# Kernel tuning notes

Hardware: AMD Instinct MI355X
Metric: run time of the kernel (lower is better)

Reference implementation:

```python
import jax, jax.numpy as jnp
import numpy as np

D = 32        # number of TT cores (d)
R = 16        # tt_rank
B = 262144    # batch size


def setup_inputs() -> dict:
    key = jax.random.key(0)
    k1, k2, k3, k4 = jax.random.split(key, 4)
    return {
        "X": jax.random.randint(k1, (B, D), 0, 2, dtype=jnp.int32),
        "core_first": jax.random.normal(k2, (1, R, 2), dtype=jnp.float32),
        "cores_mid": jax.random.normal(k3, (D - 2, R, R, 2), dtype=jnp.float32),
        "core_last": jax.random.normal(k4, (R, 1, 2), dtype=jnp.float32),
    }


def reference(X, core_first, cores_mid, core_last):
    # First core: cores[0][:, :, X[:,0]] -> [1, R, B] -> permute -> [B, 1, R].
    # We carry the squeezed [B, R] row vector instead of [B, 1, R].
    carry0 = jnp.take(core_first[0], X[:, 0], axis=-1).T  # [B, R]

    def step(carry, inp):
        core, idx = inp                       # core: [R, R, 2], idx: [B]
        c = jnp.take(core, idx, axis=2)       # gathered core: [R, R, B]
        new = jnp.einsum('br,rsb->bs', carry, c)  # batched (1xR)@(RxR)
        return new, None

    # Middle cores i = 1 .. D-2 (sequential chain, data-dependent).
    carry, _ = jax.lax.scan(step, carry0, (cores_mid, X[:, 1:D - 1].T))

    # Last core: cores[-1][:, :, X[:,-1]] -> [R, 1, B]; contract to scalar per batch.
    c_last = jnp.take(core_last[:, 0, :], X[:, -1], axis=-1)  # [R, B]
    out = jnp.einsum('br,rb->b', carry, c_last)               # [B]  (squeeze of [B,1,1])
    return out
```

## Files before the change

### kernel.cpp

```cpp
#include <hip/hip_runtime.h>


#define R 16
#define TT_D 32
#define BATCH 262144

#define OFF_V8   0
#define OFF_P8   (OFF_V8 + 4096)
#define OFF_Q8   (OFF_P8 + 65536)
#define OFF_W8   (OFF_Q8 + 65536)
#define OFF_V16  (OFF_W8 + 4096)
#define OFF_W16  (OFF_V16 + 1048576)
#define WS_FLOATS (OFF_W16 + 1048576)

typedef int   v4i __attribute__((ext_vector_type(4)));
typedef float v4f __attribute__((ext_vector_type(4)));
typedef float v2f __attribute__((ext_vector_type(2)));

__device__ inline void row_chain4(const float* __restrict__ Lc, int cbase, int e, int r,
                                  float* __restrict__ v) {
    const int b0 = (e >> 3) & 1, b1 = (e >> 2) & 1, b2 = (e >> 1) & 1, b3 = e & 1;
    #pragma unroll
    for (int s = 0; s < 16; s++) v[s] = Lc[((((cbase * 2 + b0) * 16) + s) << 4) + r];
    const int bits[3] = { b1, b2, b3 };
    #pragma unroll
    for (int k = 1; k <= 3; k++) {
        const float* M = Lc + (((cbase + k) * 2 + bits[k - 1]) << 8);
        float nv[16];
        #pragma unroll
        for (int s2 = 0; s2 < 16; s2++) {
            float acc = 0.f;
            #pragma unroll
            for (int r2 = 0; r2 < 16; r2++) acc += v[r2] * M[(s2 << 4) + r2];
            nv[s2] = acc;
        }
        #pragma unroll
        for (int s2 = 0; s2 < 16; s2++) v[s2] = nv[s2];
    }
}

__global__ __launch_bounds__(256) void tt_build1(const float* __restrict__ cf,
                                                 const float* __restrict__ cm,
                                                 const float* __restrict__ cl,
                                                 float* __restrict__ ws) {
    __shared__ float sh[12288];
    const int g = blockIdx.x;
    const int t = threadIdx.x;

    if (g < 32) {
        const bool isP = (g < 16);
        const int gb = isP ? g : g - 16;
        const int coreBase = isP ? 7 : 15;
        for (int i = t; i < 8 * 512; i += 256) {
            const int c = i >> 9, j = i & 511;
            const int x = j & 1, s = (j >> 1) & 15, r = j >> 5;
            sh[(((c * 2 + x) * 16) + s) * 16 + r] = cm[coreBase * 512 + i];
        }
        __syncthreads();
        {
            const int e = t >> 4, r = t & 15;
            float v[16];
            row_chain4(sh, 4, e, r, v);
            #pragma unroll
            for (int s = 0; s < 16; s++) sh[8192 + (e << 8) + (r << 4) + s] = v[s];
        }
        if (t < 16) {
            float v[16];
            row_chain4(sh, 0, gb, t, v);
            #pragma unroll
            for (int s = 0; s < 16; s++) sh[4096 + (t << 4) + s] = v[s];
        }
        __syncthreads();
        {
            const int l = t >> 4, r = t & 15;
            float h[16], outv[16];
            #pragma unroll
            for (int k = 0; k < 16; k++) h[k] = sh[4096 + (r << 4) + k];
            #pragma unroll
            for (int s2 = 0; s2 < 16; s2++) outv[s2] = 0.f;
            #pragma unroll
            for (int k = 0; k < 16; k++) {
                const float a = h[k];
                #pragma unroll
                for (int s2 = 0; s2 < 16; s2++) outv[s2] += a * sh[8192 + (l << 8) + (k << 4) + s2];
            }
            const int e8 = gb * 16 + l;
            float* o = ws + (isP ? OFF_P8 : OFF_Q8) + (e8 << 8) + (r << 4);
            #pragma unroll
            for (int s2 = 0; s2 < 16; s2++) o[s2] = outv[s2];
        }
    } else if (g == 32) {
        for (int i = t; i < 7 * 512; i += 256) {
            const int c = i >> 9, j = i & 511;
            const int x = j & 1, s = (j >> 1) & 15, r = j >> 5;
            sh[(((c * 2 + x) * 16) + s) * 16 + r] = cm[i];
        }
        if (t < 32) sh[8192 + t] = cf[t];
        __syncthreads();
        {
            const int e = t >> 4, r = t & 15;
            float v[16];
            row_chain4(sh, 3, e, r, v);
            #pragma unroll
            for (int s = 0; s < 16; s++) sh[4096 + (e << 8) + (r << 4) + s] = v[s];
        }
        if (t < 16) {
            const int e = t;
            const int b0 = (e >> 3) & 1, b1 = (e >> 2) & 1, b2 = (e >> 1) & 1, b3 = e & 1;
            float v[16];
            #pragma unroll
            for (int s = 0; s < 16; s++) v[s] = sh[8192 + s * 2 + b0];
            const int bits[3] = { b1, b2, b3 };
            #pragma unroll
            for (int k = 1; k <= 3; k++) {
                const float* M = sh + (((k - 1) * 2 + bits[k - 1]) << 8);
                float nv[16];
                #pragma unroll
                for (int s2 = 0; s2 < 16; s2++) {
                    float acc = 0.f;
                    #pragma unroll
                    for (int r2 = 0; r2 < 16; r2++) acc += v[r2] * M[(s2 << 4) + r2];
                    nv[s2] = acc;
                }
                #pragma unroll
                for (int s2 = 0; s2 < 16; s2++) v[s2] = nv[s2];
            }
            #pragma unroll
            for (int s = 0; s < 16; s++) sh[8256 + (e << 4) + s] = v[s];
        }
        __syncthreads();
        {
            const int h = t >> 4, l = t & 15;
            float outv[16];
            #pragma unroll
            for (int s2 = 0; s2 < 16; s2++) outv[s2] = 0.f;
            #pragma unroll
            for (int k = 0; k < 16; k++) {
                const float a = sh[8256 + (h << 4) + k];
                #pragma unroll
                for (int s2 = 0; s2 < 16; s2++) outv[s2] += a * sh[4096 + (l << 8) + (k << 4) + s2];
            }
            float* o = ws + OFF_V8 + (t << 4);
            #pragma unroll
            for (int s2 = 0; s2 < 16; s2++) o[s2] = outv[s2];
        }
    } else {
        for (int i = t; i < 7 * 512; i += 256) {
            const int c = i >> 9, j = i & 511;
            const int x = j & 1, s = (j >> 1) & 15, r = j >> 5;
            sh[(((c * 2 + x) * 16) + s) * 16 + r] = cm[23 * 512 + i];
        }
        if (t < 32) sh[8192 + t] = cl[t];
        __syncthreads();
        {
            const int e = t >> 4, r = t & 15;
            float v[16];
            row_chain4(sh, 0, e, r, v);
            #pragma unroll
            for (int s = 0; s < 16; s++) sh[4096 + (e << 8) + (r << 4) + s] = v[s];
        }
        if (t < 16) {
            const int e = t;
            const int b0 = (e >> 3) & 1, b1 = (e >> 2) & 1, b2 = (e >> 1) & 1, b3 = e & 1;
            float w[16];
            #pragma unroll
            for (int r2 = 0; r2 < 16; r2++) w[r2] = sh[8192 + r2 * 2 + b3];
            const int cidx[3] = { 6, 5, 4 };
            const int bidx[3] = { b2, b1, b0 };
            #pragma unroll
            for (int k = 0; k < 3; k++) {
                const float* M = sh + ((cidx[k] * 2 + bidx[k]) << 8);
                float nw[16];
                #pragma unroll
                for (int r2 = 0; r2 < 16; r2++) {
                    float acc = 0.f;
                    #pragma unroll
                    for (int kk = 0; kk < 16; kk++) acc += M[(kk << 4) + r2] * w[kk];
                    nw[r2] = acc;
                }
                #pragma unroll
                for (int r2 = 0; r2 < 16; r2++) w[r2] = nw[r2];
            }
            #pragma unroll
            for (int r2 = 0; r2 < 16; r2++) sh[8256 + (e << 4) + r2] = w[r2];
        }
        __syncthreads();
        {
            const int h = t >> 4, l = t & 15;
            float w4[16], outv[16];
            #pragma unroll
            for (int k = 0; k < 16; k++) w4[k] = sh[8256 + (l << 4) + k];
            #pragma unroll
            for (int r2 = 0; r2 < 16; r2++) {
                float acc = 0.f;
                #pragma unroll
                for (int k = 0; k < 16; k++) acc += sh[4096 + (h << 8) + (r2 << 4) + k] * w4[k];
                outv[r2] = acc;
            }
            float* o = ws + OFF_W8 + (t << 4);
            #pragma unroll
            for (int r2 = 0; r2 < 16; r2++) o[r2] = outv[r2];
        }
    }
}

__global__ __launch_bounds__(256) void tt_build2(float* __restrict__ ws) {
    const int t = threadIdx.x;
    if (blockIdx.x < 256) {
        const int h = blockIdx.x, l = t;
        __shared__ float sv[16];
        if (t < 16) sv[t] = ws[OFF_V8 + h * 16 + t];
        __syncthreads();
        const float* P = ws + OFF_P8 + (l << 8);
        float outv[16];
        #pragma unroll
        for (int s2 = 0; s2 < 16; s2++) outv[s2] = 0.f;
        #pragma unroll
        for (int r2 = 0; r2 < 16; r2++) {
            const float a = sv[r2];
            #pragma unroll
            for (int s2 = 0; s2 < 16; s2++) outv[s2] += a * P[(r2 << 4) + s2];
        }
        float* o = ws + OFF_V16 + (size_t)((h << 8) + l) * 16;
        #pragma unroll
        for (int s2 = 0; s2 < 16; s2++) o[s2] = outv[s2];
    } else {
        const int h = blockIdx.x - 256, l = t;
        __shared__ float sQ[256];
        sQ[t] = ws[OFF_Q8 + (h << 8) + t];
        __syncthreads();
        const float* wv = ws + OFF_W8 + (l << 4);
        float w[16];
        #pragma unroll
        for (int k = 0; k < 16; k++) w[k] = wv[k];
        float outv[16];
        #pragma unroll
        for (int r2 = 0; r2 < 16; r2++) {
            float acc = 0.f;
            #pragma unroll
            for (int k = 0; k < 16; k++) acc += sQ[(r2 << 4) + k] * w[k];
            outv[r2] = acc;
        }
        float* o = ws + OFF_W16 + (size_t)((h << 8) + l) * 16;
        #pragma unroll
        for (int r2 = 0; r2 < 16; r2++) o[r2] = outv[r2];
    }
}

__global__ __launch_bounds__(256) void tt_main2(const int* __restrict__ X,
                                                const float* __restrict__ ws,
                                                float* __restrict__ out) {
    const int tid = blockIdx.x * 256 + threadIdx.x;
    const v4i* Xr = (const v4i*)(X + (size_t)tid * 64);
    v4i c[16];
    #pragma unroll
    for (int q = 0; q < 16; q++) c[q] = __builtin_nontemporal_load(Xr + q);

    unsigned key[4] = { 0u, 0u, 0u, 0u };
    #pragma unroll
    for (int q = 0; q < 16; q++) {
        const unsigned nib = ((unsigned)(c[q].x & 1) << 3) | ((unsigned)(c[q].y & 1) << 2) |
                             ((unsigned)(c[q].z & 1) << 1) | (unsigned)(c[q].w & 1);
        key[q >> 2] = (key[q >> 2] << 4) | nib;
    }

    const v4f* v0 = (const v4f*)(ws + OFF_V16 + (size_t)key[0] * 16);
    const v4f* w0 = (const v4f*)(ws + OFF_W16 + (size_t)key[1] * 16);
    const v4f* v1 = (const v4f*)(ws + OFF_V16 + (size_t)key[2] * 16);
    const v4f* w1 = (const v4f*)(ws + OFF_W16 + (size_t)key[3] * 16);

    v4f acc0 = { 0.f, 0.f, 0.f, 0.f }, acc1 = { 0.f, 0.f, 0.f, 0.f };
    #pragma unroll
    for (int k = 0; k < 4; k++) acc0 += v0[k] * w0[k];
    #pragma unroll
    for (int k = 0; k < 4; k++) acc1 += v1[k] * w1[k];

    v2f res;
    res.x = acc0.x + acc0.y + acc0.z + acc0.w;
    res.y = acc1.x + acc1.y + acc1.z + acc1.w;
    __builtin_nontemporal_store(res, (v2f*)(out + (size_t)tid * 2));
}

__global__ __launch_bounds__(256) void tt_direct(const int* __restrict__ X,
                                                 const float* __restrict__ cf,
                                                 const float* __restrict__ cm,
                                                 const float* __restrict__ cl,
                                                 float* __restrict__ out) {
    __shared__ float scm[30 * 16 * 16 * 2];
    for (int i = threadIdx.x; i < 30 * 16 * 16 * 2; i += blockDim.x) scm[i] = cm[i];
    __syncthreads();
    const int b = blockIdx.x * blockDim.x + threadIdx.x;
    if (b >= BATCH) return;
    const int* xr = X + (size_t)b * TT_D;
    float v[R], nv[R];
    const int x0 = xr[0] & 1;
    #pragma unroll
    for (int r = 0; r < R; r++) v[r] = cf[r * 2 + x0];
    for (int i = 1; i <= 30; i++) {
        const int bit = xr[i] & 1;
        const float* M = scm + (i - 1) * 512;
        #pragma unroll
        for (int s2 = 0; s2 < R; s2++) {
            float acc = 0.f;
            #pragma unroll
            for (int r = 0; r < R; r++) acc += v[r] * M[(r * 16 + s2) * 2 + bit];
            nv[s2] = acc;
        }
        #pragma unroll
        for (int s2 = 0; s2 < R; s2++) v[s2] = nv[s2];
    }
    const int xl = xr[31] & 1;
    float acc = 0.f;
    #pragma unroll
    for (int r = 0; r < R; r++) acc += v[r] * cl[r * 2 + xl];
    out[b] = acc;
}

extern "C" void kernel_launch(void* const* d_in, const int* in_sizes, int n_in,
                              void* d_out, int out_size, void* d_ws, size_t ws_size,
                              hipStream_t stream) {
    const int* X = (const int*)d_in[0];
    const float* cf = (const float*)d_in[1];
    const float* cm = (const float*)d_in[2];
    const float* cl = (const float*)d_in[3];
    float* out = (float*)d_out;

    if (ws_size >= (size_t)WS_FLOATS * sizeof(float)) {
        float* ws = (float*)d_ws;
        tt_build1<<<34, 256, 0, stream>>>(cf, cm, cl, ws);
        tt_build2<<<512, 256, 0, stream>>>(ws);
        tt_main2<<<BATCH / 512, 256, 0, stream>>>(X, ws, out);
    } else {
        tt_direct<<<(BATCH + 255) / 256, 256, 0, stream>>>(X, cf, cm, cl, out);
    }
}
```

Before: 135.1 us.

## Rebuild 8-core byte tables with one block per table entry

The table-building stage moves from 34 large blocks, each doing serial nibble chains in a big shared buffer, to 544 small blocks. Each block computes one 8-core product directly as a chain of 16x16 matrix steps, one thread per output element, reading cores straight from global memory. The second stage is rearranged so each block holds one P matrix in shared memory and loops over the V8 vectors. The aim is to shorten the latency of the build phase by filling more compute units, at the cost of more redundant global reads and a barrier at every chain step.

```diff
diff --git a/kernel.cpp b/kernel.cpp
--- a/kernel.cpp
+++ b/kernel.cpp
@@ -17,233 +17,124 @@
 typedef float v4f __attribute__((ext_vector_type(4)));
 typedef float v2f __attribute__((ext_vector_type(2)));
 
-__device__ inline void row_chain4(const float* __restrict__ Lc, int cbase, int e, int r,
-                                  float* __restrict__ v) {
-    const int b0 = (e >> 3) & 1, b1 = (e >> 2) & 1, b2 = (e >> 1) & 1, b3 = e & 1;
-    #pragma unroll
-    for (int s = 0; s < 16; s++) v[s] = Lc[((((cbase * 2 + b0) * 16) + s) << 4) + r];
-    const int bits[3] = { b1, b2, b3 };
-    #pragma unroll
-    for (int k = 1; k <= 3; k++) {
-        const float* M = Lc + (((cbase + k) * 2 + bits[k - 1]) << 8);
-        float nv[16];
-        #pragma unroll
-        for (int s2 = 0; s2 < 16; s2++) {
-            float acc = 0.f;
-            #pragma unroll
-            for (int r2 = 0; r2 < 16; r2++) acc += v[r2] * M[(s2 << 4) + r2];
-            nv[s2] = acc;
-        }
-        #pragma unroll
-        for (int s2 = 0; s2 < 16; s2++) v[s2] = nv[s2];
-    }
-}
-
-__global__ __launch_bounds__(256) void tt_build1(const float* __restrict__ cf,
-                                                 const float* __restrict__ cm,
-                                                 const float* __restrict__ cl,
-                                                 float* __restrict__ ws) {
-    __shared__ float sh[12288];
+__global__ __launch_bounds__(256) void tt_byte_build(const float* __restrict__ cf,
+                                                     const float* __restrict__ cm,
+                                                     const float* __restrict__ cl,
+                                                     float* __restrict__ ws) {
+    __shared__ float sA[256], sB[256];
     const int g = blockIdx.x;
     const int t = threadIdx.x;
 
-    if (g < 32) {
-        const bool isP = (g < 16);
-        const int gb = isP ? g : g - 16;
-        const int coreBase = isP ? 7 : 15;
-        for (int i = t; i < 8 * 512; i += 256) {
-            const int c = i >> 9, j = i & 511;
-            const int x = j & 1, s = (j >> 1) & 15, r = j >> 5;
-            sh[(((c * 2 + x) * 16) + s) * 16 + r] = cm[coreBase * 512 + i];
-        }
-        __syncthreads();
+    if (g < 512) {
+        const bool isP = (g < 256);
+        const int e = g & 255;
+        const int base = isP ? 7 : 15;
+        const int r = t >> 4, s = t & 15;
         {
-            const int e = t >> 4, r = t & 15;
-            float v[16];
-            row_chain4(sh, 4, e, r, v);
-            #pragma unroll
-            for (int s = 0; s < 16; s++) sh[8192 + (e << 8) + (r << 4) + s] = v[s];
-        }
-        if (t < 16) {
-            float v[16];
-            row_chain4(sh, 0, gb, t, v);
-            #pragma unroll
-            for (int s = 0; s < 16; s++) sh[4096 + (t << 4) + s] = v[s];
-        }
-        __syncthreads();
-        {
-            const int l = t >> 4, r = t & 15;
-            float h[16], outv[16];
-            #pragma unroll
-            for (int k = 0; k < 16; k++) h[k] = sh[4096 + (r << 4) + k];
-            #pragma unroll
-            for (int s2 = 0; s2 < 16; s2++) outv[s2] = 0.f;
-            #pragma unroll
-            for (int k = 0; k < 16; k++) {
-                const float a = h[k];
-                #pragma unroll
-                for (int s2 = 0; s2 < 16; s2++) outv[s2] += a * sh[8192 + (l << 8) + (k << 4) + s2];
-            }
-            const int e8 = gb * 16 + l;
-            float* o = ws + (isP ? OFF_P8 : OFF_Q8) + (e8 << 8) + (r << 4);
-            #pragma unroll
-            for (int s2 = 0; s2 < 16; s2++) o[s2] = outv[s2];
-        }
-    } else if (g == 32) {
-        for (int i = t; i < 7 * 512; i += 256) {
-            const int c = i >> 9, j = i & 511;
-            const int x = j & 1, s = (j >> 1) & 15, r = j >> 5;
-            sh[(((c * 2 + x) * 16) + s) * 16 + r] = cm[i];
-        }
-        if (t < 32) sh[8192 + t] = cf[t];
-        __syncthreads();
-        {
-            const int e = t >> 4, r = t & 15;
-            float v[16];
-            row_chain4(sh, 3, e, r, v);
-            #pragma unroll
-            for (int s = 0; s < 16; s++) sh[4096 + (e << 8) + (r << 4) + s] = v[s];
-        }
-        if (t < 16) {
-            const int e = t;
-            const int b0 = (e >> 3) & 1, b1 = (e >> 2) & 1, b2 = (e >> 1) & 1, b3 = e & 1;
-            float v[16];
-            #pragma unroll
-            for (int s = 0; s < 16; s++) v[s] = sh[8192 + s * 2 + b0];
-            const int bits[3] = { b1, b2, b3 };
-            #pragma unroll
-            for (int k = 1; k <= 3; k++) {
-                const float* M = sh + (((k - 1) * 2 + bits[k - 1]) << 8);
-                float nv[16];
-                #pragma unroll
-                for (int s2 = 0; s2 < 16; s2++) {
-                    float acc = 0.f;
-                    #pragma unroll
-                    for (int r2 = 0; r2 < 16; r2++) acc += v[r2] * M[(s2 << 4) + r2];
-                    nv[s2] = acc;
-                }
-                #pragma unroll
-                for (int s2 = 0; s2 < 16; s2++) v[s2] = nv[s2];
-            }
-            #pragma unroll
-            for (int s = 0; s < 16; s++) sh[8256 + (e << 4) + s] = v[s];
-        }
-        __syncthreads();
-        {
-            const int h = t >> 4, l = t & 15;
-            float outv[16];
-            #pragma unroll
-            for (int s2 = 0; s2 < 16; s2++) outv[s2] = 0.f;
-            #pragma unroll
-            for (int k = 0; k < 16; k++) {
-                const float a = sh[8256 + (h << 4) + k];
-                #pragma unroll
-                for (int s2 = 0; s2 < 16; s2++) outv[s2] += a * sh[4096 + (l << 8) + (k << 4) + s2];
-            }
-            float* o = ws + OFF_V8 + (t << 4);
-            #pragma unroll
-            for (int s2 = 0; s2 < 16; s2++) o[s2] = outv[s2];
-        }
+            const int b = (e >> 7) & 1;
+            sA[t] = cm[(((base * 16 + r) * 16) + s) * 2 + b];
+        }
+        float* cur = sA; float* nxt = sB;
+        float acc = 0.f;
+        for (int j = 1; j < 8; j++) {
+            __syncthreads();
+            const int b = (e >> (7 - j)) & 1;
+            const float* M = cm + (base + j) * 512 + b;
+            acc = 0.f;
+            #pragma unroll
+            for (int k = 0; k < 16; k++)
+                acc += cur[r * 16 + k] * M[(k * 16 + s) * 2];
+            nxt[t] = acc;
+            float* tmp = cur; cur = nxt; nxt = tmp;
+        }
+        ws[(isP ? OFF_P8 : OFF_Q8) + (e << 8) + t] = acc;
+    } else if (g < 528) {
+        const int eb = (g - 512) * 16;
+        const int el = t >> 4, s = t & 15;
+        const int e = eb + el;
+        sA[t] = cf[s * 2 + ((e >> 7) & 1)];
+        float* cur = sA; float* nxt = sB;
+        float acc = 0.f;
+        for (int j = 0; j < 7; j++) {
+            __syncthreads();
+            const int b = (e >> (6 - j)) & 1;
+            const float* M = cm + j * 512 + b;
+            acc = 0.f;
+            #pragma unroll
+            for (int r2 = 0; r2 < 16; r2++)
+                acc += cur[el * 16 + r2] * M[(r2 * 16 + s) * 2];
+            nxt[t] = acc;
+            float* tmp = cur; cur = nxt; nxt = tmp;
+        }
+        ws[OFF_V8 + eb * 16 + t] = acc;
     } else {
-        for (int i = t; i < 7 * 512; i += 256) {
-            const int c = i >> 9, j = i & 511;
-            const int x = j & 1, s = (j >> 1) & 15, r = j >> 5;
-            sh[(((c * 2 + x) * 16) + s) * 16 + r] = cm[23 * 512 + i];
-        }
-        if (t < 32) sh[8192 + t] = cl[t];
-        __syncthreads();
-        {
-            const int e = t >> 4, r = t & 15;
-            float v[16];
-            row_chain4(sh, 0, e, r, v);
-            #pragma unroll
-            for (int s = 0; s < 16; s++) sh[4096 + (e << 8) + (r << 4) + s] = v[s];
-        }
-        if (t < 16) {
-            const int e = t;
-            const int b0 = (e >> 3) & 1, b1 = (e >> 2) & 1, b2 = (e >> 1) & 1, b3 = e & 1;
-            float w[16];
-            #pragma unroll
-            for (int r2 = 0; r2 < 16; r2++) w[r2] = sh[8192 + r2 * 2 + b3];
-            const int cidx[3] = { 6, 5, 4 };
-            const int bidx[3] = { b2, b1, b0 };
-            #pragma unroll
-            for (int k = 0; k < 3; k++) {
-                const float* M = sh + ((cidx[k] * 2 + bidx[k]) << 8);
-                float nw[16];
-                #pragma unroll
-                for (int r2 = 0; r2 < 16; r2++) {
-                    float acc = 0.f;
-                    #pragma unroll
-                    for (int kk = 0; kk < 16; kk++) acc += M[(kk << 4) + r2] * w[kk];
-                    nw[r2] = acc;
-                }
-                #pragma unroll
-                for (int r2 = 0; r2 < 16; r2++) w[r2] = nw[r2];
-            }
-            #pragma unroll
-            for (int r2 = 0; r2 < 16; r2++) sh[8256 + (e << 4) + r2] = w[r2];
-        }
-        __syncthreads();
-        {
-            const int h = t >> 4, l = t & 15;
-            float w4[16], outv[16];
-            #pragma unroll
-            for (int k = 0; k < 16; k++) w4[k] = sh[8256 + (l << 4) + k];
-            #pragma unroll
-            for (int r2 = 0; r2 < 16; r2++) {
-                float acc = 0.f;
-                #pragma unroll
-                for (int k = 0; k < 16; k++) acc += sh[4096 + (h << 8) + (r2 << 4) + k] * w4[k];
-                outv[r2] = acc;
-            }
-            float* o = ws + OFF_W8 + (t << 4);
-            #pragma unroll
-            for (int r2 = 0; r2 < 16; r2++) o[r2] = outv[r2];
-        }
-    }
-}
-
-__global__ __launch_bounds__(256) void tt_build2(float* __restrict__ ws) {
+        const int eb = (g - 528) * 16;
+        const int el = t >> 4, r = t & 15;
+        const int e = eb + el;
+        sA[t] = cl[r * 2 + (e & 1)];
+        float* cur = sA; float* nxt = sB;
+        float acc = 0.f;
+        for (int j = 0; j < 7; j++) {
+            __syncthreads();
+            const int c = 29 - j;
+            const int b = (e >> (1 + j)) & 1;
+            const float* M = cm + c * 512 + b;
+            acc = 0.f;
+            #pragma unroll
+            for (int k = 0; k < 16; k++)
+                acc += M[(r * 16 + k) * 2] * cur[el * 16 + k];
+            nxt[t] = acc;
+            float* tmp = cur; cur = nxt; nxt = tmp;
+        }
+        ws[OFF_W8 + eb * 16 + t] = acc;
+    }
+}
+
+__global__ __launch_bounds__(256) void tt_tab(float* __restrict__ ws) {
     const int t = threadIdx.x;
     if (blockIdx.x < 256) {
-        const int h = blockIdx.x, l = t;
-        __shared__ float sv[16];
-        if (t < 16) sv[t] = ws[OFF_V8 + h * 16 + t];
+        const int l = blockIdx.x;
+        __shared__ float sP[256];
+        sP[t] = ws[OFF_P8 + (l << 8) + t];
         __syncthreads();
-        const float* P = ws + OFF_P8 + (l << 8);
-        float outv[16];
-        #pragma unroll
-        for (int s2 = 0; s2 < 16; s2++) outv[s2] = 0.f;
-        #pragma unroll
-        for (int r2 = 0; r2 < 16; r2++) {
-            const float a = sv[r2];
-            #pragma unroll
-            for (int s2 = 0; s2 < 16; s2++) outv[s2] += a * P[(r2 << 4) + s2];
-        }
-        float* o = ws + OFF_V16 + (size_t)((h << 8) + l) * 16;
-        #pragma unroll
-        for (int s2 = 0; s2 < 16; s2++) o[s2] = outv[s2];
+        const int h = t;
+        const float* v8 = ws + OFF_V8 + (h << 4);
+        float v[16];
+        #pragma unroll
+        for (int k = 0; k < 16; k++) v[k] = v8[k];
+        float o[16];
+        #pragma unroll
+        for (int s = 0; s < 16; s++) o[s] = 0.f;
+        #pragma unroll
+        for (int r = 0; r < 16; r++) {
+            const float a = v[r];
+            #pragma unroll
+            for (int s = 0; s < 16; s++) o[s] += a * sP[r * 16 + s];
+        }
+        float* dst = ws + OFF_V16 + ((size_t)((h << 8) | l) << 4);
+        #pragma unroll
+        for (int s = 0; s < 16; s++) dst[s] = o[s];
     } else {
-        const int h = blockIdx.x - 256, l = t;
+        const int h = blockIdx.x - 256;
         __shared__ float sQ[256];
         sQ[t] = ws[OFF_Q8 + (h << 8) + t];
         __syncthreads();
-        const float* wv = ws + OFF_W8 + (l << 4);
+        const int l = t;
+        const float* w8 = ws + OFF_W8 + (l << 4);
         float w[16];
         #pragma unroll
-        for (int k = 0; k < 16; k++) w[k] = wv[k];
-        float outv[16];
-        #pragma unroll
-        for (int r2 = 0; r2 < 16; r2++) {
+        for (int k = 0; k < 16; k++) w[k] = w8[k];
+        float o[16];
+        #pragma unroll
+        for (int r = 0; r < 16; r++) {
             float acc = 0.f;
             #pragma unroll
-            for (int k = 0; k < 16; k++) acc += sQ[(r2 << 4) + k] * w[k];
-            outv[r2] = acc;
-        }
-        float* o = ws + OFF_W16 + (size_t)((h << 8) + l) * 16;
-        #pragma unroll
-        for (int r2 = 0; r2 < 16; r2++) o[r2] = outv[r2];
+            for (int k = 0; k < 16; k++) acc += sQ[r * 16 + k] * w[k];
+            o[r] = acc;
+        }
+        float* dst = ws + OFF_W16 + ((size_t)((h << 8) | l) << 4);
+        #pragma unroll
+        for (int r = 0; r < 16; r++) dst[r] = o[r];
     }
 }
 
@@ -327,8 +218,8 @@
 
     if (ws_size >= (size_t)WS_FLOATS * sizeof(float)) {
         float* ws = (float*)d_ws;
-        tt_build1<<<34, 256, 0, stream>>>(cf, cm, cl, ws);
-        tt_build2<<<512, 256, 0, stream>>>(ws);
+        tt_byte_build<<<544, 256, 0, stream>>>(cf, cm, cl, ws);
+        tt_tab<<<512, 256, 0, stream>>>(ws);
         tt_main2<<<BATCH / 512, 256, 0, stream>>>(X, ws, out);
     } else {
         tt_direct<<<(BATCH + 255) / 256, 256, 0, stream>>>(X, cf, cm, cl, out);
```

Result: faster. 129.2 us (-4.4%).
